# Kernel optimization log

Hardware: AMD Instinct MI355X
Metric: run time of the kernel (lower is better)

## Reference

```python
import jax, jax.numpy as jnp
import numpy as np
import math

D = 128      # out_dim (= d)
H = 4        # n_heads
DK = D // H  # d_k = 32
M = 5        # fixed num types in forward
NN = 15      # fixed N in forward
SQRT_DK = math.sqrt(DK)


def setup_inputs() -> dict:
    key = jax.random.key(0)
    ks = jax.random.split(key, 18)
    b, n = 1024, 64
    inp = {
        "node_inp": jax.random.normal(ks[0], (D, b, n), jnp.float32),
        "WW": jax.random.normal(ks[1], (b, M, n, NN), jnp.float32) * 0.1,
        "mask_matrix": jax.random.uniform(ks[2], (M * NN, n), jnp.float32),
        "R": jax.random.normal(ks[3], (b, H, n, n), jnp.float32),
        "attn_mask": jax.random.uniform(ks[4], (1, 1, n, 4 * n), jnp.float32),
        # learned parameters (xavier-ish scale)
        "WK": jax.random.normal(ks[5], (M, D, D), jnp.float32) * 0.05,
        "bK": jax.random.normal(ks[6], (M, D, 1), jnp.float32) * 0.05,
        "WQ": jax.random.normal(ks[7], (M, D, D), jnp.float32) * 0.05,
        "bQ": jax.random.normal(ks[8], (M, D, 1), jnp.float32) * 0.05,
        "WM": jax.random.normal(ks[9], (M, D, D), jnp.float32) * 0.05,
        "bM": jax.random.normal(ks[10], (M, D, 1), jnp.float32) * 0.05,
        "WB": jax.random.normal(ks[11], (M, D, D), jnp.float32) * 0.05,
        "bB": jax.random.normal(ks[12], (M, D, 1), jnp.float32) * 0.05,
        "Wmsgup": jax.random.normal(ks[13], (DK, DK), jnp.float32) * 0.1,
        "Wmsgdown": jax.random.normal(ks[14], (DK, DK), jnp.float32) * 0.1,
        "Wmsgleft": jax.random.normal(ks[15], (DK, DK), jnp.float32) * 0.1,
        "Wmsgright": jax.random.normal(ks[16], (DK, DK), jnp.float32) * 0.1,
    }
    return inp


def reference(node_inp, WW, mask_matrix, R, attn_mask,
              WK, bK, WQ, bQ, WM, bM, WB, bB,
              Wmsgup, Wmsgdown, Wmsgleft, Wmsgright):
    d, b, n = node_inp.shape
    # project node features through per-type mixing: (b, m, d, N)
    node_inp_m = jnp.einsum('dbn,bmnN->bmdN', node_inp, WW)

    def proj_perm(W, bias):
        # per-type linear then permute(0,2,1,3) before flatten (as K/Q do)
        x = jnp.einsum('mde,bmeN->bmdN', W, node_inp_m) + bias[None]  # (b,m,d,N)
        x = x.transpose(0, 2, 1, 3).reshape(b, d, M * NN)
        return x @ mask_matrix  # (b, d, n)

    K = proj_perm(WK, bK).reshape(b, H, DK, n)
    Q = proj_perm(WQ, bQ).reshape(b, H, DK, n)

    # message: NOTE original reshapes (b*m,d,N) -> (b,d,m*N) WITHOUT the permute; replicate faithfully
    msg = jnp.einsum('mde,bmeN->bmdN', WM, node_inp_m) + bM[None]  # (b,m,d,N)
    message = msg.reshape(b, d, M * NN) @ mask_matrix               # (b, d, n)

    A = jnp.einsum('bhki,bhkj->bhij', Q, K) / SQRT_DK               # (b,h,n,n)
    aw = jax.nn.softmax(R + A, axis=3)
    aw = jnp.where(jnp.isnan(aw), jnp.zeros_like(aw), aw)
    aw = jnp.tile(aw, (1, 1, 1, 4)) * attn_mask                     # (b,h,n,4n)

    res_msg = message.reshape(b, H, DK, n)
    Wmsg = jnp.concatenate([Wmsgup, Wmsgdown, Wmsgleft, Wmsgright], axis=1)  # (dk, 4dk)
    res = jnp.einsum('kq,bhkn->bhqn', Wmsg, res_msg)                # (b,h,4dk,n)
    res = res.reshape(b, H, DK, 4 * n)                               # faithful reshape

    B = jnp.einsum('bhnm,bhkm->bhkn', aw, res).reshape(b, d, n)
    B = jax.nn.gelu(B, approximate=False)

    Bm = jnp.einsum('bdn,bmnN->bmdN', B, WW)
    Bm = jnp.einsum('mde,bmeN->bmdN', WB, Bm) + bB[None]
    Bm = Bm.transpose(0, 2, 1, 3).reshape(b, d, M * NN) @ mask_matrix  # (b,d,n)
    out = Bm.transpose(1, 0, 2) + node_inp                             # (d,b,n)
    return (out, aw[0, 0])
```

## Files before the change

### kernel.cpp

```cpp
#include <hip/hip_runtime.h>
#include <math.h>

#define Dd 128
#define Hh 4
#define DKk 32
#define Mm 5
#define NNn 15
#define Bb 1024
#define Nn 64
#define MN 75
#define BN 65536
#define RSQRT_DK 0.17677669529663687f

typedef __attribute__((ext_vector_type(8))) short bf16x8;
typedef __attribute__((ext_vector_type(4))) float f32x4;

__device__ __forceinline__ ushort f2bf(float x) {
    unsigned u = __float_as_uint(x);
    u = (u + 0x7fffu + ((u >> 16) & 1u)) >> 16;
    return (ushort)u;
}
__device__ __forceinline__ float bf2f(ushort h) {
    return __uint_as_float(((unsigned)h) << 16);
}
__device__ __forceinline__ void split2(float x, ushort& hi, ushort& lo) {
    hi = f2bf(x);
    lo = f2bf(x - bf2f(hi));
}
__device__ __forceinline__ f32x4 MFMA(bf16x8 a, bf16x8 b, f32x4 c) {
    return __builtin_amdgcn_mfma_f32_16x16x32_bf16(a, b, c, 0, 0, 0);
}

__global__ void k0_prep(const float* __restrict__ maskm,
                        const float* __restrict__ WK, const float* __restrict__ bK,
                        const float* __restrict__ WQ, const float* __restrict__ bQ,
                        const float* __restrict__ WM, const float* __restrict__ bM,
                        const float* __restrict__ WB, const float* __restrict__ bB,
                        const float* __restrict__ Wu, const float* __restrict__ Wd,
                        const float* __restrict__ Wl, const float* __restrict__ Wr,
                        ushort* __restrict__ WKhi, ushort* __restrict__ WKlo,
                        ushort* __restrict__ WQhi, ushort* __restrict__ WQlo,
                        ushort* __restrict__ WMhi, ushort* __restrict__ WBhi,
                        ushort* __restrict__ maskhi, ushort* __restrict__ masklo,
                        ushort* __restrict__ maskThi, ushort* __restrict__ maskTlo,
                        float* __restrict__ btKT, float* __restrict__ btQT,
                        float* __restrict__ btMT, float* __restrict__ btB,
                        ushort* __restrict__ WcatT)
{
    int tid = blockIdx.x * blockDim.x + threadIdx.x;
    int nthr = gridDim.x * blockDim.x;
    const int NW = Mm * Dd * Dd;
    for (int i = tid; i < NW; i += nthr) {
        split2(WK[i], WKhi[i], WKlo[i]);
        split2(WQ[i], WQhi[i], WQlo[i]);
        WMhi[i] = f2bf(WM[i]);
        WBhi[i] = f2bf(WB[i]);
    }
    for (int i = tid; i < 96 * 64; i += nthr) {
        float v = (i < MN * 64) ? maskm[i] : 0.f;
        split2(v, maskhi[i], masklo[i]);
    }
    for (int i = tid; i < 64 * 96; i += nthr) {
        int col = i / 96, j = i - col * 96;
        float v = (j < MN) ? maskm[j * 64 + col] : 0.f;
        split2(v, maskThi[i], maskTlo[i]);
    }
    for (int i = tid; i < 4096; i += nthr) {
        int q = i >> 5, kk = i & 31;
        const float* Wsel = (q < 32) ? Wu : (q < 64) ? Wd : (q < 96) ? Wl : Wr;
        WcatT[i] = f2bf(Wsel[kk * 32 + (q & 31)]);
    }
    for (int i = tid; i < 8192; i += nthr) {
        int d = i >> 6, col = i & 63;
        float aKv = 0.f, aQv = 0.f, aBv = 0.f;
        for (int m = 0; m < Mm; ++m) {
            float mrs = 0.f;
            for (int N = 0; N < NNn; ++N) mrs += maskm[(m * 15 + N) * 64 + col];
            aKv += bK[m * 128 + d] * mrs;
            aQv += bQ[m * 128 + d] * mrs;
            aBv += bB[m * 128 + d] * mrs;
        }
        btKT[col * 128 + d] = aKv;
        btQT[col * 128 + d] = aQv;
        btB[i] = aBv;
        float aMv = 0.f;
        for (int j = 0; j < MN; ++j) {
            int f = d * 75 + j;
            int m = f / 1920;
            int dloc = (f / 15) & 127;
            aMv += bM[m * 128 + dloc] * maskm[j * 64 + col];
        }
        btMT[col * 128 + d] = aMv;
    }
}

__global__ __launch_bounds__(512, 4) void k1_proj(
    const float* __restrict__ node, const float* __restrict__ WW,
    const ushort* __restrict__ WKhi, const ushort* __restrict__ WKlo,
    const ushort* __restrict__ WQhi, const ushort* __restrict__ WQlo,
    const ushort* __restrict__ WMhi,
    const ushort* __restrict__ maskThi, const ushort* __restrict__ maskTlo,
    const float* __restrict__ btKT, const float* __restrict__ btQT,
    const float* __restrict__ btMT,
    ushort* __restrict__ Khi, ushort* __restrict__ Klo,
    ushort* __restrict__ Qhi, ushort* __restrict__ Qlo,
    ushort* __restrict__ msgTg)
{
    const int b = blockIdx.x;
    const int tid = threadIdx.x;
    const int lane = tid & 63, w = tid >> 6;
    const int l15 = lane & 15, lq = lane >> 4;

    __shared__ ushort nimTh[80 * 136];
    __shared__ ushort nimTl[80 * 136];
    __shared__ ushort planes[4 * 32 * 104];

    ushort* Ykh = planes;
    ushort* Ykl = planes + 32 * 104;
    ushort* Yqh = planes + 2 * 32 * 104;
    ushort* Yql = planes + 3 * 32 * 104;

    for (int t = tid; t < 5 * 136; t += 512) {
        int mm = t / 136, e = t - mm * 136;
        nimTh[(mm * 16 + 15) * 136 + e] = 0;
        nimTl[(mm * 16 + 15) * 136 + e] = 0;
    }
    for (int t = tid; t < 128 * 29; t += 512) {
        int r = t / 29, cc = 75 + (t - r * 29);
        planes[r * 104 + cc] = 0;
    }

    const f32x4 zz = {0.f, 0.f, 0.f, 0.f};

    {
        bf16x8 ah[2], al[2];
        #pragma unroll
        for (int ks = 0; ks < 2; ++ks) {
            const float* np = node + (size_t)(w * 16 + l15) * BN + b * 64 + ks * 32 + lq * 8;
            float tmp[8];
            *(float4*)tmp       = *(const float4*)np;
            *(float4*)(tmp + 4) = *(const float4*)(np + 4);
            #pragma unroll
            for (int j = 0; j < 8; ++j) {
                ushort h_, l_; split2(tmp[j], h_, l_);
                ah[ks][j] = (short)h_; al[ks][j] = (short)l_;
            }
        }
        for (int m = 0; m < Mm; ++m) {
            const float* wp = WW + ((size_t)b * Mm + m) * 960 + (l15 < 15 ? l15 : 0);
            f32x4 chh = zz, chl = zz, clh = zz;
            #pragma unroll
            for (int ks = 0; ks < 2; ++ks) {
                bf16x8 bh, bl;
                #pragma unroll
                for (int t = 0; t < 8; ++t) {
                    int n = ks * 32 + lq * 8 + t;
                    float v = (l15 < 15) ? wp[n * 15] : 0.f;
                    ushort h_, l_; split2(v, h_, l_);
                    bh[t] = (short)h_; bl[t] = (short)l_;
                }
                chh = MFMA(ah[ks], bh, chh);
                chl = MFMA(ah[ks], bl, chl);
                clh = MFMA(al[ks], bh, clh);
            }
            f32x4 c = chh + chl + clh;
            if (l15 < 15) {
                #pragma unroll
                for (int t = 0; t < 4; ++t) {
                    int e = w * 16 + lq * 4 + t;
                    split2(c[t], nimTh[(m * 16 + l15) * 136 + e],
                                 nimTl[(m * 16 + l15) * 136 + e]);
                }
            }
        }
    }
    __syncthreads();

    for (int qd = 0; qd < 4; ++qd) {
        for (int u = w; u < 10; u += 8) {
            int m = u >> 1, rt = u & 1;
            int d0 = qd * 32 + rt * 16 + l15;
            f32x4 khh = zz, khl = zz, klh = zz;
            f32x4 qhh = zz, qhl = zz, qlh = zz;
            #pragma unroll
            for (int ks = 0; ks < 4; ++ks) {
                int k0 = ks * 32 + lq * 8;
                size_t wo = (size_t)m * 16384 + (size_t)d0 * 128 + k0;
                bf16x8 akh = *(const bf16x8*)(WKhi + wo);
                bf16x8 akl = *(const bf16x8*)(WKlo + wo);
                bf16x8 aqh = *(const bf16x8*)(WQhi + wo);
                bf16x8 aql = *(const bf16x8*)(WQlo + wo);
                bf16x8 bh = *(const bf16x8*)(&nimTh[(m * 16 + l15) * 136 + k0]);
                bf16x8 bl = *(const bf16x8*)(&nimTl[(m * 16 + l15) * 136 + k0]);
                khh = MFMA(akh, bh, khh); khl = MFMA(akh, bl, khl); klh = MFMA(akl, bh, klh);
                qhh = MFMA(aqh, bh, qhh); qhl = MFMA(aqh, bl, qhl); qlh = MFMA(aql, bh, qlh);
            }
            f32x4 cK = khh + khl + klh;
            f32x4 cQ = qhh + qhl + qlh;
            if (l15 < 15) {
                int j = m * 15 + l15;
                #pragma unroll
                for (int t = 0; t < 4; ++t) {
                    int r = rt * 16 + lq * 4 + t;
                    split2(cK[t], Ykh[r * 104 + j], Ykl[r * 104 + j]);
                    split2(cQ[t], Yqh[r * 104 + j], Yql[r * 104 + j]);
                }
            }
        }
        __syncthreads();
        {
            int nr = w & 3, dc = w >> 2;
            f32x4 khh = zz, khl = zz, klh = zz;
            f32x4 qhh = zz, qhl = zz, qlh = zz;
            #pragma unroll
            for (int ks = 0; ks < 3; ++ks) {
                int k0 = ks * 32 + lq * 8;
                bf16x8 mh = *(const bf16x8*)(maskThi + (nr * 16 + l15) * 96 + k0);
                bf16x8 ml = *(const bf16x8*)(maskTlo + (nr * 16 + l15) * 96 + k0);
                bf16x8 ykh = *(const bf16x8*)(&Ykh[(dc * 16 + l15) * 104 + k0]);
                bf16x8 ykl = *(const bf16x8*)(&Ykl[(dc * 16 + l15) * 104 + k0]);
                bf16x8 yqh = *(const bf16x8*)(&Yqh[(dc * 16 + l15) * 104 + k0]);
                bf16x8 yql = *(const bf16x8*)(&Yql[(dc * 16 + l15) * 104 + k0]);
                khh = MFMA(mh, ykh, khh); khl = MFMA(ml, ykh, khl); klh = MFMA(mh, ykl, klh);
                qhh = MFMA(mh, yqh, qhh); qhl = MFMA(ml, yqh, qhl); qlh = MFMA(mh, yql, qlh);
            }
            f32x4 cK = khh + khl + klh;
            f32x4 cQ = qhh + qhl + qlh;
            #pragma unroll
            for (int t = 0; t < 4; ++t) {
                int n = nr * 16 + lq * 4 + t;
                int dloc = dc * 16 + l15;
                int d = qd * 32 + dloc;
                size_t oi = (((size_t)(b * 4 + qd)) * 64 + n) * 32 + dloc;
                ushort hh_, ll_;
                split2(cK[t] + btKT[n * 128 + d], hh_, ll_);
                Khi[oi] = hh_; Klo[oi] = ll_;
                split2(cQ[t] + btQT[n * 128 + d], hh_, ll_);
                Qhi[oi] = hh_; Qlo[oi] = ll_;
            }
        }
        __syncthreads();
    }

    {
        int rt = w;
        for (int m = 0; m < Mm; ++m) {
            f32x4 c0 = zz, c1 = zz;
            #pragma unroll
            for (int ks = 0; ks < 4; ++ks) {
                int k0 = ks * 32 + lq * 8;
                bf16x8 a  = *(const bf16x8*)(WMhi + (size_t)m * 16384 + (size_t)(rt * 16 + l15) * 128 + k0);
                bf16x8 bh = *(const bf16x8*)(&nimTh[(m * 16 + l15) * 136 + k0]);
                if (ks < 2) c0 = MFMA(a, bh, c0); else c1 = MFMA(a, bh, c1);
            }
            f32x4 c = c0 + c1;
            if (l15 < 15) {
                #pragma unroll
                for (int t = 0; t < 4; ++t) {
                    int dflat = rt * 16 + lq * 4 + t;
                    int g = m * 1920 + dflat * 15 + l15;
                    planes[(g / 75) * 104 + (g % 75)] = f2bf(c[t]);
                }
            }
        }
    }
    __syncthreads();
    #pragma unroll
    for (int s = 0; s < 4; ++s) {
        int u = w * 4 + s;
        int nr = u & 3, ddc = u >> 2;
        f32x4 cs0 = zz, cs1 = zz, cs2 = zz;
        {
            bf16x8 a0 = *(const bf16x8*)(maskThi + (nr * 16 + l15) * 96 + lq * 8);
            bf16x8 b0 = *(const bf16x8*)(&planes[(ddc * 16 + l15) * 104 + lq * 8]);
            cs0 = MFMA(a0, b0, cs0);
            bf16x8 a1 = *(const bf16x8*)(maskThi + (nr * 16 + l15) * 96 + 32 + lq * 8);
            bf16x8 b1 = *(const bf16x8*)(&planes[(ddc * 16 + l15) * 104 + 32 + lq * 8]);
            cs1 = MFMA(a1, b1, cs1);
            bf16x8 a2 = *(const bf16x8*)(maskThi + (nr * 16 + l15) * 96 + 64 + lq * 8);
            bf16x8 b2 = *(const bf16x8*)(&planes[(ddc * 16 + l15) * 104 + 64 + lq * 8]);
            cs2 = MFMA(a2, b2, cs2);
        }
        f32x4 c = cs0 + cs1 + cs2;
        #pragma unroll
        for (int t = 0; t < 4; ++t) {
            int n = nr * 16 + lq * 4 + t;
            int dd = ddc * 16 + l15;
            int h = dd >> 5, dk = dd & 31;
            msgTg[(((size_t)(b * 4 + h)) * 64 + n) * 32 + dk] = f2bf(c[t] + btMT[n * 128 + dd]);
        }
    }
}

__global__ __launch_bounds__(512, 4) void k2_attn(
    const ushort* __restrict__ Khi, const ushort* __restrict__ Klo,
    const ushort* Qhi, const ushort* __restrict__ Qlo,
    const ushort* __restrict__ msgTg,
    const float* __restrict__ R, const float* __restrict__ am,
    const ushort* __restrict__ WcatT, float* __restrict__ aw00,
    ushort* Bout)
{
    const int b = blockIdx.x >> 2, h = blockIdx.x & 3;
    const int tid = threadIdx.x;
    const int lane = tid & 63, w = tid >> 6;
    const int l15 = lane & 15, lq = lane >> 4;

    __shared__ float  ST[64 * 65];
    __shared__ ushort resS[128 * 72];
    __shared__ ushort awq[64 * 72];

    const f32x4 zz = {0.f, 0.f, 0.f, 0.f};
    const size_t base2 = (size_t)(b * 4 + h) * 2048;
    const float* Rb = R + (size_t)(b * 4 + h) * 4096;

    {
        int ti = w >> 1;
        bf16x8 ah = *(const bf16x8*)(Qhi + base2 + (size_t)(ti * 16 + l15) * 32 + lq * 8);
        bf16x8 al = *(const bf16x8*)(Qlo + base2 + (size_t)(ti * 16 + l15) * 32 + lq * 8);
        #pragma unroll
        for (int s = 0; s < 2; ++s) {
            int tj = (w & 1) * 2 + s;
            bf16x8 bh = *(const bf16x8*)(Khi + base2 + (size_t)(tj * 16 + l15) * 32 + lq * 8);
            bf16x8 bl = *(const bf16x8*)(Klo + base2 + (size_t)(tj * 16 + l15) * 32 + lq * 8);
            f32x4 chh = zz, chl = zz, clh = zz;
            chh = MFMA(ah, bh, chh); chl = MFMA(ah, bl, chl); clh = MFMA(al, bh, clh);
            f32x4 c = chh + chl + clh;
            #pragma unroll
            for (int r = 0; r < 4; ++r) {
                int i = ti * 16 + lq * 4 + r, j = tj * 16 + l15;
                ST[j * 65 + i] = Rb[i * 64 + j] + c[r] * RSQRT_DK;
            }
        }
    }
    {
        bf16x8 a = *(const bf16x8*)(WcatT + (w * 16 + l15) * 32 + lq * 8);
        #pragma unroll
        for (int nt = 0; nt < 4; ++nt) {
            bf16x8 bfr = *(const bf16x8*)(msgTg + base2 + (size_t)(nt * 16 + l15) * 32 + lq * 8);
            f32x4 c = MFMA(a, bfr, zz);
            #pragma unroll
            for (int r = 0; r < 4; ++r)
                resS[(w * 16 + lq * 4 + r) * 72 + nt * 16 + l15] = f2bf(c[r]);
        }
    }
    __syncthreads();

    {
        int row = tid >> 3, part = tid & 7;
        float v[8]; float mx = -INFINITY;
        #pragma unroll
        for (int jj = 0; jj < 8; ++jj) { v[jj] = ST[(part * 8 + jj) * 65 + row]; mx = fmaxf(mx, v[jj]); }
        mx = fmaxf(mx, __shfl_xor(mx, 1));
        mx = fmaxf(mx, __shfl_xor(mx, 2));
        mx = fmaxf(mx, __shfl_xor(mx, 4));
        float s = 0.f;
        #pragma unroll
        for (int jj = 0; jj < 8; ++jj) { v[jj] = expf(v[jj] - mx); s += v[jj]; }
        s += __shfl_xor(s, 1); s += __shfl_xor(s, 2); s += __shfl_xor(s, 4);
        float inv = 1.f / s;
        #pragma unroll
        for (int jj = 0; jj < 8; ++jj) {
            float p = v[jj] * inv;
            ST[(part * 8 + jj) * 65 + row] = isnan(p) ? 0.f : p;
        }
    }
    __syncthreads();

    const int kt = w >> 2, it = w & 3;
    f32x4 accB0 = zz, accB1 = zz;
    for (int q = 0; q < 4; ++q) {
        for (int e = tid; e < 4096; e += 512) {
            int i = e >> 6, j0 = e & 63;
            float p = ST[j0 * 65 + i] * am[i * 256 + q * 64 + j0];
            awq[i * 72 + j0] = f2bf(p);
            if (blockIdx.x == 0) aw00[i * 256 + q * 64 + j0] = p;
        }
        __syncthreads();
        int row = 4 * (kt * 16 + l15) + q;
        bf16x8 a0 = *(const bf16x8*)(&resS[row * 72 + lq * 8]);
        bf16x8 b0 = *(const bf16x8*)(&awq[(it * 16 + l15) * 72 + lq * 8]);
        accB0 = MFMA(a0, b0, accB0);
        bf16x8 a1 = *(const bf16x8*)(&resS[row * 72 + 32 + lq * 8]);
        bf16x8 b1 = *(const bf16x8*)(&awq[(it * 16 + l15) * 72 + 32 + lq * 8]);
        accB1 = MFMA(a1, b1, accB1);
        __syncthreads();
    }
    f32x4 accB = accB0 + accB1;

    #pragma unroll
    for (int r = 0; r < 4; ++r) {
        int k = kt * 16 + lq * 4 + r, i = it * 16 + l15;
        float x = accB[r];
        float g = 0.5f * x * (1.f + erff(x * 0.70710678118654752f));
        Bout[base2 + k * 64 + i] = f2bf(g);
    }
}

__global__ __launch_bounds__(512, 4) void k3_out(
    const ushort* Bbuf, const float* __restrict__ WW,
    const ushort* __restrict__ WBhi, const ushort* __restrict__ maskhi,
    const float* __restrict__ btB, const float* __restrict__ node,
    float* __restrict__ outp)
{
    const int b = blockIdx.x, tid = threadIdx.x;
    const int lane = tid & 63, w = tid >> 6, l15 = lane & 15, lq = lane >> 4;
    __shared__ ushort sB[128 * 72];
    __shared__ ushort wwh[64 * 17];
    __shared__ ushort t1[128 * 17];
    __shared__ ushort nm[32 * 66];

    for (int i = tid; i < 8192; i += 512) {
        int d = i >> 6, n = i & 63;
        sB[d * 72 + n] = Bbuf[(size_t)b * 8192 + i];
    }
    const f32x4 zz = {0.f, 0.f, 0.f, 0.f};
    f32x4 acc[4];
    for (int c = 0; c < 4; ++c) acc[c] = zz;
    __syncthreads();

    for (int m = 0; m < Mm; ++m) {
        for (int i = tid; i < 64 * 17; i += 512) {
            int n = i / 17, N = i - n * 17;
            wwh[i] = (N < 15) ? f2bf(WW[(((size_t)b * Mm + m) * 64 + n) * 15 + N]) : (ushort)0;
        }
        __syncthreads();
        {
            f32x4 c0 = zz, c1 = zz;
            #pragma unroll
            for (int ks = 0; ks < 2; ++ks) {
                int k0 = ks * 32 + (lq << 3);
                bf16x8 a = *(const bf16x8*)(&sB[(w * 16 + l15) * 72 + k0]);
                bf16x8 bh;
                #pragma unroll
                for (int t = 0; t < 8; ++t) bh[t] = (short)wwh[(k0 + t) * 17 + l15];
                if (ks == 0) c0 = MFMA(a, bh, c0); else c1 = MFMA(a, bh, c1);
            }
            f32x4 c = c0 + c1;
            #pragma unroll
            for (int t = 0; t < 4; ++t)
                t1[(w * 16 + lq * 4 + t) * 17 + l15] = f2bf(c[t]);
        }
        __syncthreads();

        bf16x8 mfh;
        {
            int ct = w & 3;
            int k0 = lq << 3;
            #pragma unroll
            for (int t = 0; t < 8; ++t) {
                int kk = k0 + t;
                int row = (kk < 15) ? (m * 15 + kk) : 95;
                mfh[t] = (short)maskhi[row * 64 + ct * 16 + l15];
            }
        }
        for (int eb = 0; eb < 4; ++eb) {
            {
                int rtl = w >> 2, ct = w & 3;
                int e = eb * 32 + rtl * 16 + l15;
                int k0 = lq << 3;
                bf16x8 a;
                #pragma unroll
                for (int t = 0; t < 8; ++t) {
                    int kk = k0 + t;
                    int cc = (kk < 15) ? kk : 15;
                    a[t] = (short)t1[e * 17 + cc];
                }
                f32x4 c = zz;
                c = MFMA(a, mfh, c);
                #pragma unroll
                for (int t = 0; t < 4; ++t)
                    nm[(rtl * 16 + lq * 4 + t) * 66 + ct * 16 + l15] = f2bf(c[t]);
            }
            __syncthreads();
            {
                size_t aoff = (size_t)(w * 16 + l15) * 128 + eb * 32 + (lq << 3);
                bf16x8 a = *(const bf16x8*)(WBhi + m * 16384 + aoff);
                int k0 = lq << 3;
                #pragma unroll
                for (int ct = 0; ct < 4; ++ct) {
                    bf16x8 bh;
                    #pragma unroll
                    for (int t = 0; t < 8; ++t) bh[t] = (short)nm[(k0 + t) * 66 + ct * 16 + l15];
                    acc[ct] = MFMA(a, bh, acc[ct]);
                }
            }
            __syncthreads();
        }
    }
    #pragma unroll
    for (int ct = 0; ct < 4; ++ct) {
        #pragma unroll
        for (int t = 0; t < 4; ++t) {
            int d = w * 16 + lq * 4 + t;
            int col = ct * 16 + l15;
            size_t gi = (size_t)d * BN + b * 64 + col;
            outp[gi] = acc[ct][t] + btB[d * 64 + col] + node[gi];
        }
    }
}

extern "C" void kernel_launch(void* const* d_in, const int* in_sizes, int n_in,
                              void* d_out, int out_size, void* d_ws, size_t ws_size,
                              hipStream_t stream) {
    const float* node  = (const float*)d_in[0];
    const float* WW    = (const float*)d_in[1];
    const float* maskm = (const float*)d_in[2];
    const float* R     = (const float*)d_in[3];
    const float* am    = (const float*)d_in[4];
    const float* WK = (const float*)d_in[5];  const float* bK = (const float*)d_in[6];
    const float* WQ = (const float*)d_in[7];  const float* bQ = (const float*)d_in[8];
    const float* WM = (const float*)d_in[9];  const float* bM = (const float*)d_in[10];
    const float* WB = (const float*)d_in[11]; const float* bB = (const float*)d_in[12];
    const float* Wu = (const float*)d_in[13]; const float* Wd = (const float*)d_in[14];
    const float* Wl = (const float*)d_in[15]; const float* Wr = (const float*)d_in[16];

    float* out  = (float*)d_out;
    float* aw00 = out + (size_t)Dd * BN;

    ushort* Khi = (ushort*)d_out;
    ushort* Klo = Khi + 8388608;

    char* W = (char*)d_ws;
    ushort* Qhi   = (ushort*)W;
    ushort* Qlo   = Qhi + 8388608;
    ushort* msgTg = Qlo + 8388608;
    ushort* WKhi  = msgTg + 8388608;
    ushort* WKlo  = WKhi + 81920;
    ushort* WQhi  = WKlo + 81920;
    ushort* WQlo  = WQhi + 81920;
    ushort* WMhi  = WQlo + 81920;
    ushort* WBhi  = WMhi + 81920;
    ushort* maskhi  = WBhi + 81920;
    ushort* masklo  = maskhi + 6144;
    ushort* maskThi = masklo + 6144;
    ushort* maskTlo = maskThi + 6144;
    ushort* WcatT   = maskTlo + 6144;
    float*  btKT = (float*)(WcatT + 4096);
    float*  btQT = btKT + 8192;
    float*  btMT = btQT + 8192;
    float*  btB  = btMT + 8192;

    k0_prep<<<512, 256, 0, stream>>>(maskm, WK, bK, WQ, bQ, WM, bM, WB, bB,
                                     Wu, Wd, Wl, Wr,
                                     WKhi, WKlo, WQhi, WQlo, WMhi, WBhi,
                                     maskhi, masklo, maskThi, maskTlo,
                                     btKT, btQT, btMT, btB, WcatT);
    k1_proj<<<Bb, 512, 0, stream>>>(node, WW, WKhi, WKlo, WQhi, WQlo, WMhi,
                                    maskThi, maskTlo, btKT, btQT, btMT,
                                    Khi, Klo, Qhi, Qlo, msgTg);
    k2_attn<<<Bb * Hh, 512, 0, stream>>>(Khi, Klo, Qhi, Qlo, msgTg, R, am,
                                         WcatT, aw00, Qhi );
    k3_out<<<Bb, 512, 0, stream>>>(Qhi , WW, WBhi, maskhi, btB, node, out);
}
```

Before: 279.7 us.

## Shrink k1 LDS footprint via swizzle, serialized K/Q passes, and buffer reuse

Reduces k1_proj shared memory by replacing padded node tiles with XOR-swizzled 128-wide rows, computing K and Q in two separate passes so only one pair of Y planes is needed, and reusing the low-half node buffer for the message plane. The launch bound is raised from 4 to 6 blocks per CU to exploit the lower LDS and register pressure. The cost is doubled passes with extra barriers and re-reading nimT tiles for Q, plus possible register spills under the tighter bound.

```diff
diff --git a/kernel.cpp b/kernel.cpp
--- a/kernel.cpp
+++ b/kernel.cpp
@@ -30,6 +30,8 @@
 __device__ __forceinline__ f32x4 MFMA(bf16x8 a, bf16x8 b, f32x4 c) {
     return __builtin_amdgcn_mfma_f32_16x16x32_bf16(a, b, c, 0, 0, 0);
 }
+
+#define NSWZ(r, c) ((r) * 128 + ((c) ^ (((r) & 7) << 3)))
 
 __global__ void k0_prep(const float* __restrict__ maskm,
                         const float* __restrict__ WK, const float* __restrict__ bK,
@@ -94,7 +96,7 @@
     }
 }
 
-__global__ __launch_bounds__(512, 4) void k1_proj(
+__global__ __launch_bounds__(512, 6) void k1_proj(
     const float* __restrict__ node, const float* __restrict__ WW,
     const ushort* __restrict__ WKhi, const ushort* __restrict__ WKlo,
     const ushort* __restrict__ WQhi, const ushort* __restrict__ WQlo,
@@ -111,26 +113,24 @@
     const int lane = tid & 63, w = tid >> 6;
     const int l15 = lane & 15, lq = lane >> 4;
 
-    __shared__ ushort nimTh[80 * 136];
-    __shared__ ushort nimTl[80 * 136];
-    __shared__ ushort planes[4 * 32 * 104];
-
-    ushort* Ykh = planes;
-    ushort* Ykl = planes + 32 * 104;
-    ushort* Yqh = planes + 2 * 32 * 104;
-    ushort* Yql = planes + 3 * 32 * 104;
-
-    for (int t = tid; t < 5 * 136; t += 512) {
-        int mm = t / 136, e = t - mm * 136;
-        nimTh[(mm * 16 + 15) * 136 + e] = 0;
-        nimTl[(mm * 16 + 15) * 136 + e] = 0;
-    }
-    for (int t = tid; t < 128 * 29; t += 512) {
+    __shared__ ushort nimTh[80 * 128];
+    __shared__ ushort nimTl[80 * 128];
+    __shared__ ushort Yh[32 * 104];
+    __shared__ ushort Yl[32 * 104];
+    ushort* xM = nimTl;
+
+    const f32x4 zz = {0.f, 0.f, 0.f, 0.f};
+
+    for (int t = tid; t < 5 * 128; t += 512) {
+        int mm = t >> 7, e = t & 127;
+        nimTh[(mm * 16 + 15) * 128 + e] = 0;
+        nimTl[(mm * 16 + 15) * 128 + e] = 0;
+    }
+    for (int t = tid; t < 32 * 29; t += 512) {
         int r = t / 29, cc = 75 + (t - r * 29);
-        planes[r * 104 + cc] = 0;
-    }
-
-    const f32x4 zz = {0.f, 0.f, 0.f, 0.f};
+        Yh[r * 104 + cc] = 0;
+        Yl[r * 104 + cc] = 0;
+    }
 
     {
         bf16x8 ah[2], al[2];
@@ -165,83 +165,83 @@
             }
             f32x4 c = chh + chl + clh;
             if (l15 < 15) {
+                int row = m * 16 + l15;
                 #pragma unroll
                 for (int t = 0; t < 4; ++t) {
                     int e = w * 16 + lq * 4 + t;
-                    split2(c[t], nimTh[(m * 16 + l15) * 136 + e],
-                                 nimTl[(m * 16 + l15) * 136 + e]);
+                    split2(c[t], nimTh[NSWZ(row, e)], nimTl[NSWZ(row, e)]);
                 }
             }
         }
     }
     __syncthreads();
 
-    for (int qd = 0; qd < 4; ++qd) {
-        for (int u = w; u < 10; u += 8) {
-            int m = u >> 1, rt = u & 1;
-            int d0 = qd * 32 + rt * 16 + l15;
-            f32x4 khh = zz, khl = zz, klh = zz;
-            f32x4 qhh = zz, qhl = zz, qlh = zz;
-            #pragma unroll
-            for (int ks = 0; ks < 4; ++ks) {
-                int k0 = ks * 32 + lq * 8;
-                size_t wo = (size_t)m * 16384 + (size_t)d0 * 128 + k0;
-                bf16x8 akh = *(const bf16x8*)(WKhi + wo);
-                bf16x8 akl = *(const bf16x8*)(WKlo + wo);
-                bf16x8 aqh = *(const bf16x8*)(WQhi + wo);
-                bf16x8 aql = *(const bf16x8*)(WQlo + wo);
-                bf16x8 bh = *(const bf16x8*)(&nimTh[(m * 16 + l15) * 136 + k0]);
-                bf16x8 bl = *(const bf16x8*)(&nimTl[(m * 16 + l15) * 136 + k0]);
-                khh = MFMA(akh, bh, khh); khl = MFMA(akh, bl, khl); klh = MFMA(akl, bh, klh);
-                qhh = MFMA(aqh, bh, qhh); qhl = MFMA(aqh, bl, qhl); qlh = MFMA(aql, bh, qlh);
-            }
-            f32x4 cK = khh + khl + klh;
-            f32x4 cQ = qhh + qhl + qlh;
-            if (l15 < 15) {
-                int j = m * 15 + l15;
+    for (int P = 0; P < 2; ++P) {
+        const ushort* Whi = P ? WQhi : WKhi;
+        const ushort* Wlo = P ? WQlo : WKlo;
+        const float*  btP = P ? btQT : btKT;
+        ushort* Phi = P ? Qhi : Khi;
+        ushort* Plo = P ? Qlo : Klo;
+
+        for (int qd = 0; qd < 4; ++qd) {
+            for (int u = w; u < 10; u += 8) {
+                int m = u >> 1, rt = u & 1;
+                int d0 = qd * 32 + rt * 16 + l15;
+                f32x4 phh = zz, phl = zz, plh = zz;
+                #pragma unroll
+                for (int ks = 0; ks < 4; ++ks) {
+                    int k0 = ks * 32 + lq * 8;
+                    size_t wo = (size_t)m * 16384 + (size_t)d0 * 128 + k0;
+                    bf16x8 awh = *(const bf16x8*)(Whi + wo);
+                    bf16x8 awl = *(const bf16x8*)(Wlo + wo);
+                    int nrow = m * 16 + l15;
+                    bf16x8 bh = *(const bf16x8*)(&nimTh[NSWZ(nrow, k0)]);
+                    bf16x8 bl = *(const bf16x8*)(&nimTl[NSWZ(nrow, k0)]);
+                    phh = MFMA(awh, bh, phh); phl = MFMA(awh, bl, phl); plh = MFMA(awl, bh, plh);
+                }
+                f32x4 c = phh + phl + plh;
+                if (l15 < 15) {
+                    int j = m * 15 + l15;
+                    #pragma unroll
+                    for (int t = 0; t < 4; ++t) {
+                        int r = rt * 16 + lq * 4 + t;
+                        split2(c[t], Yh[r * 104 + j], Yl[r * 104 + j]);
+                    }
+                }
+            }
+            __syncthreads();
+            {
+                int nr = w & 3, dc = w >> 2;
+                f32x4 phh = zz, phl = zz, plh = zz;
+                #pragma unroll
+                for (int ks = 0; ks < 3; ++ks) {
+                    int k0 = ks * 32 + lq * 8;
+                    bf16x8 mh = *(const bf16x8*)(maskThi + (nr * 16 + l15) * 96 + k0);
+                    bf16x8 ml = *(const bf16x8*)(maskTlo + (nr * 16 + l15) * 96 + k0);
+                    bf16x8 yh = *(const bf16x8*)(&Yh[(dc * 16 + l15) * 104 + k0]);
+                    bf16x8 yl = *(const bf16x8*)(&Yl[(dc * 16 + l15) * 104 + k0]);
+                    phh = MFMA(mh, yh, phh); phl = MFMA(ml, yh, phl); plh = MFMA(mh, yl, plh);
+                }
+                f32x4 c = phh + phl + plh;
                 #pragma unroll
                 for (int t = 0; t < 4; ++t) {
-                    int r = rt * 16 + lq * 4 + t;
-                    split2(cK[t], Ykh[r * 104 + j], Ykl[r * 104 + j]);
-                    split2(cQ[t], Yqh[r * 104 + j], Yql[r * 104 + j]);
-                }
-            }
-        }
-        __syncthreads();
-        {
-            int nr = w & 3, dc = w >> 2;
-            f32x4 khh = zz, khl = zz, klh = zz;
-            f32x4 qhh = zz, qhl = zz, qlh = zz;
-            #pragma unroll
-            for (int ks = 0; ks < 3; ++ks) {
-                int k0 = ks * 32 + lq * 8;
-                bf16x8 mh = *(const bf16x8*)(maskThi + (nr * 16 + l15) * 96 + k0);
-                bf16x8 ml = *(const bf16x8*)(maskTlo + (nr * 16 + l15) * 96 + k0);
-                bf16x8 ykh = *(const bf16x8*)(&Ykh[(dc * 16 + l15) * 104 + k0]);
-                bf16x8 ykl = *(const bf16x8*)(&Ykl[(dc * 16 + l15) * 104 + k0]);
-                bf16x8 yqh = *(const bf16x8*)(&Yqh[(dc * 16 + l15) * 104 + k0]);
-                bf16x8 yql = *(const bf16x8*)(&Yql[(dc * 16 + l15) * 104 + k0]);
-                khh = MFMA(mh, ykh, khh); khl = MFMA(ml, ykh, khl); klh = MFMA(mh, ykl, klh);
-                qhh = MFMA(mh, yqh, qhh); qhl = MFMA(ml, yqh, qhl); qlh = MFMA(mh, yql, qlh);
-            }
-            f32x4 cK = khh + khl + klh;
-            f32x4 cQ = qhh + qhl + qlh;
-            #pragma unroll
-            for (int t = 0; t < 4; ++t) {
-                int n = nr * 16 + lq * 4 + t;
-                int dloc = dc * 16 + l15;
-                int d = qd * 32 + dloc;
-                size_t oi = (((size_t)(b * 4 + qd)) * 64 + n) * 32 + dloc;
-                ushort hh_, ll_;
-                split2(cK[t] + btKT[n * 128 + d], hh_, ll_);
-                Khi[oi] = hh_; Klo[oi] = ll_;
-                split2(cQ[t] + btQT[n * 128 + d], hh_, ll_);
-                Qhi[oi] = hh_; Qlo[oi] = ll_;
-            }
-        }
-        __syncthreads();
-    }
-
+                    int n = nr * 16 + lq * 4 + t;
+                    int dloc = dc * 16 + l15;
+                    int d = qd * 32 + dloc;
+                    size_t oi = (((size_t)(b * 4 + qd)) * 64 + n) * 32 + dloc;
+                    ushort hh_, ll_;
+                    split2(c[t] + btP[n * 128 + d], hh_, ll_);
+                    Phi[oi] = hh_; Plo[oi] = ll_;
+                }
+            }
+            __syncthreads();
+        }
+    }
+
+    for (int t = tid; t < 128 * 5; t += 512) {
+        int r = t / 5, cc = 75 + (t - r * 5);
+        xM[r * 80 + cc] = 0;
+    }
     {
         int rt = w;
         for (int m = 0; m < Mm; ++m) {
@@ -250,7 +250,8 @@
             for (int ks = 0; ks < 4; ++ks) {
                 int k0 = ks * 32 + lq * 8;
                 bf16x8 a  = *(const bf16x8*)(WMhi + (size_t)m * 16384 + (size_t)(rt * 16 + l15) * 128 + k0);
-                bf16x8 bh = *(const bf16x8*)(&nimTh[(m * 16 + l15) * 136 + k0]);
+                int nrow = m * 16 + l15;
+                bf16x8 bh = *(const bf16x8*)(&nimTh[NSWZ(nrow, k0)]);
                 if (ks < 2) c0 = MFMA(a, bh, c0); else c1 = MFMA(a, bh, c1);
             }
             f32x4 c = c0 + c1;
@@ -259,7 +260,7 @@
                 for (int t = 0; t < 4; ++t) {
                     int dflat = rt * 16 + lq * 4 + t;
                     int g = m * 1920 + dflat * 15 + l15;
-                    planes[(g / 75) * 104 + (g % 75)] = f2bf(c[t]);
+                    xM[(g / 75) * 80 + (g % 75)] = f2bf(c[t]);
                 }
             }
         }
@@ -272,13 +273,13 @@
         f32x4 cs0 = zz, cs1 = zz, cs2 = zz;
         {
             bf16x8 a0 = *(const bf16x8*)(maskThi + (nr * 16 + l15) * 96 + lq * 8);
-            bf16x8 b0 = *(const bf16x8*)(&planes[(ddc * 16 + l15) * 104 + lq * 8]);
+            bf16x8 b0 = *(const bf16x8*)(&xM[(ddc * 16 + l15) * 80 + lq * 8]);
             cs0 = MFMA(a0, b0, cs0);
             bf16x8 a1 = *(const bf16x8*)(maskThi + (nr * 16 + l15) * 96 + 32 + lq * 8);
-            bf16x8 b1 = *(const bf16x8*)(&planes[(ddc * 16 + l15) * 104 + 32 + lq * 8]);
+            bf16x8 b1 = *(const bf16x8*)(&xM[(ddc * 16 + l15) * 80 + 32 + lq * 8]);
             cs1 = MFMA(a1, b1, cs1);
             bf16x8 a2 = *(const bf16x8*)(maskThi + (nr * 16 + l15) * 96 + 64 + lq * 8);
-            bf16x8 b2 = *(const bf16x8*)(&planes[(ddc * 16 + l15) * 104 + 64 + lq * 8]);
+            bf16x8 b2 = *(const bf16x8*)(&xM[(ddc * 16 + l15) * 80 + 64 + lq * 8]);
             cs2 = MFMA(a2, b2, cs2);
         }
         f32x4 c = cs0 + cs1 + cs2;
```

New measurement: 319.2 us. 14.1% more time.

## Split projection kernel into nim, K/Q, and message kernels via global staging

Applied to the files above, without the earlier changes.

The monolithic per-batch projection kernel is split into three kernels. The first computes the WW-mixed node features and stores their hi/lo bf16 parts to a new global workspace. The second computes K/Q with one block per (batch, quarter), giving four times more blocks and smaller LDS use. The third computes the message projection. This is meant to raise occupancy and parallelism and shrink per-block LDS, at the cost of a large global round trip for the intermediate features (about 40 MB) and two extra launches.

```diff
diff --git a/kernel.cpp b/kernel.cpp
--- a/kernel.cpp
+++ b/kernel.cpp
@@ -94,49 +94,28 @@
     }
 }
 
-__global__ __launch_bounds__(512, 4) void k1_proj(
+__global__ __launch_bounds__(256, 6) void k1a_nim(
     const float* __restrict__ node, const float* __restrict__ WW,
-    const ushort* __restrict__ WKhi, const ushort* __restrict__ WKlo,
-    const ushort* __restrict__ WQhi, const ushort* __restrict__ WQlo,
-    const ushort* __restrict__ WMhi,
-    const ushort* __restrict__ maskThi, const ushort* __restrict__ maskTlo,
-    const float* __restrict__ btKT, const float* __restrict__ btQT,
-    const float* __restrict__ btMT,
-    ushort* __restrict__ Khi, ushort* __restrict__ Klo,
-    ushort* __restrict__ Qhi, ushort* __restrict__ Qlo,
-    ushort* __restrict__ msgTg)
+    ushort* __restrict__ nimHg, ushort* __restrict__ nimLg)
 {
     const int b = blockIdx.x;
     const int tid = threadIdx.x;
     const int lane = tid & 63, w = tid >> 6;
     const int l15 = lane & 15, lq = lane >> 4;
-
-    __shared__ ushort nimTh[80 * 136];
-    __shared__ ushort nimTl[80 * 136];
-    __shared__ ushort planes[4 * 32 * 104];
-
-    ushort* Ykh = planes;
-    ushort* Ykl = planes + 32 * 104;
-    ushort* Yqh = planes + 2 * 32 * 104;
-    ushort* Yql = planes + 3 * 32 * 104;
-
-    for (int t = tid; t < 5 * 136; t += 512) {
-        int mm = t / 136, e = t - mm * 136;
-        nimTh[(mm * 16 + 15) * 136 + e] = 0;
-        nimTl[(mm * 16 + 15) * 136 + e] = 0;
-    }
-    for (int t = tid; t < 128 * 29; t += 512) {
-        int r = t / 29, cc = 75 + (t - r * 29);
-        planes[r * 104 + cc] = 0;
-    }
-
     const f32x4 zz = {0.f, 0.f, 0.f, 0.f};
 
-    {
+    for (int t = tid; t < 5 * 128; t += 256) {
+        int mm = t >> 7, e = t & 127;
+        nimHg[(size_t)b * 10240 + (mm * 16 + 15) * 128 + e] = 0;
+        nimLg[(size_t)b * 10240 + (mm * 16 + 15) * 128 + e] = 0;
+    }
+
+    for (int s = 0; s < 2; ++s) {
+        int eb = w * 2 + s;
         bf16x8 ah[2], al[2];
         #pragma unroll
         for (int ks = 0; ks < 2; ++ks) {
-            const float* np = node + (size_t)(w * 16 + l15) * BN + b * 64 + ks * 32 + lq * 8;
+            const float* np = node + (size_t)(eb * 16 + l15) * BN + b * 64 + ks * 32 + lq * 8;
             float tmp[8];
             *(float4*)tmp       = *(const float4*)np;
             *(float4*)(tmp + 4) = *(const float4*)(np + 4);
@@ -165,92 +144,143 @@
             }
             f32x4 c = chh + chl + clh;
             if (l15 < 15) {
-                #pragma unroll
-                for (int t = 0; t < 4; ++t) {
-                    int e = w * 16 + lq * 4 + t;
-                    split2(c[t], nimTh[(m * 16 + l15) * 136 + e],
-                                 nimTl[(m * 16 + l15) * 136 + e]);
-                }
+                int row = m * 16 + l15;
+                ushort h0, h1, h2, h3, l0, l1, l2, l3;
+                split2(c[0], h0, l0); split2(c[1], h1, l1);
+                split2(c[2], h2, l2); split2(c[3], h3, l3);
+                size_t base = (size_t)b * 10240 + row * 128 + eb * 16 + lq * 4;
+                *(unsigned*)(nimHg + base)     = (unsigned)h0 | ((unsigned)h1 << 16);
+                *(unsigned*)(nimHg + base + 2) = (unsigned)h2 | ((unsigned)h3 << 16);
+                *(unsigned*)(nimLg + base)     = (unsigned)l0 | ((unsigned)l1 << 16);
+                *(unsigned*)(nimLg + base + 2) = (unsigned)l2 | ((unsigned)l3 << 16);
+            }
+        }
+    }
+}
+
+__global__ __launch_bounds__(256, 6) void k1b_kq(
+    const ushort* __restrict__ nimHg, const ushort* __restrict__ nimLg,
+    const ushort* __restrict__ WKhi, const ushort* __restrict__ WKlo,
+    const ushort* __restrict__ WQhi, const ushort* __restrict__ WQlo,
+    const ushort* __restrict__ maskThi, const ushort* __restrict__ maskTlo,
+    const float* __restrict__ btKT, const float* __restrict__ btQT,
+    ushort* __restrict__ Khi, ushort* __restrict__ Klo,
+    ushort* __restrict__ Qhi, ushort* __restrict__ Qlo)
+{
+    const int b = blockIdx.x >> 2, qd = blockIdx.x & 3;
+    const int tid = threadIdx.x;
+    const int lane = tid & 63, w = tid >> 6;
+    const int l15 = lane & 15, lq = lane >> 4;
+
+    __shared__ ushort Ykh[32 * 104], Ykl[32 * 104];
+    __shared__ ushort Yqh[32 * 104], Yql[32 * 104];
+
+    const f32x4 zz = {0.f, 0.f, 0.f, 0.f};
+    const size_t nbase = (size_t)b * 10240;
+
+    for (int t = tid; t < 32 * 29; t += 256) {
+        int r = t / 29, cc = 75 + (t - r * 29);
+        Ykh[r * 104 + cc] = 0; Ykl[r * 104 + cc] = 0;
+        Yqh[r * 104 + cc] = 0; Yql[r * 104 + cc] = 0;
+    }
+
+    for (int u = w; u < 10; u += 4) {
+        int m = u >> 1, rt = u & 1;
+        int d0 = qd * 32 + rt * 16 + l15;
+        f32x4 khh = zz, khl = zz, klh = zz;
+        f32x4 qhh = zz, qhl = zz, qlh = zz;
+        #pragma unroll
+        for (int ks = 0; ks < 4; ++ks) {
+            int k0 = ks * 32 + lq * 8;
+            size_t wo = (size_t)m * 16384 + (size_t)d0 * 128 + k0;
+            bf16x8 akh = *(const bf16x8*)(WKhi + wo);
+            bf16x8 akl = *(const bf16x8*)(WKlo + wo);
+            bf16x8 aqh = *(const bf16x8*)(WQhi + wo);
+            bf16x8 aql = *(const bf16x8*)(WQlo + wo);
+            bf16x8 bh = *(const bf16x8*)(nimHg + nbase + (m * 16 + l15) * 128 + k0);
+            bf16x8 bl = *(const bf16x8*)(nimLg + nbase + (m * 16 + l15) * 128 + k0);
+            khh = MFMA(akh, bh, khh); khl = MFMA(akh, bl, khl); klh = MFMA(akl, bh, klh);
+            qhh = MFMA(aqh, bh, qhh); qhl = MFMA(aqh, bl, qhl); qlh = MFMA(aql, bh, qlh);
+        }
+        f32x4 cK = khh + khl + klh;
+        f32x4 cQ = qhh + qhl + qlh;
+        if (l15 < 15) {
+            int j = m * 15 + l15;
+            #pragma unroll
+            for (int t = 0; t < 4; ++t) {
+                int r = rt * 16 + lq * 4 + t;
+                split2(cK[t], Ykh[r * 104 + j], Ykl[r * 104 + j]);
+                split2(cQ[t], Yqh[r * 104 + j], Yql[r * 104 + j]);
             }
         }
     }
     __syncthreads();
 
-    for (int qd = 0; qd < 4; ++qd) {
-        for (int u = w; u < 10; u += 8) {
-            int m = u >> 1, rt = u & 1;
-            int d0 = qd * 32 + rt * 16 + l15;
-            f32x4 khh = zz, khl = zz, klh = zz;
-            f32x4 qhh = zz, qhl = zz, qlh = zz;
-            #pragma unroll
-            for (int ks = 0; ks < 4; ++ks) {
-                int k0 = ks * 32 + lq * 8;
-                size_t wo = (size_t)m * 16384 + (size_t)d0 * 128 + k0;
-                bf16x8 akh = *(const bf16x8*)(WKhi + wo);
-                bf16x8 akl = *(const bf16x8*)(WKlo + wo);
-                bf16x8 aqh = *(const bf16x8*)(WQhi + wo);
-                bf16x8 aql = *(const bf16x8*)(WQlo + wo);
-                bf16x8 bh = *(const bf16x8*)(&nimTh[(m * 16 + l15) * 136 + k0]);
-                bf16x8 bl = *(const bf16x8*)(&nimTl[(m * 16 + l15) * 136 + k0]);
-                khh = MFMA(akh, bh, khh); khl = MFMA(akh, bl, khl); klh = MFMA(akl, bh, klh);
-                qhh = MFMA(aqh, bh, qhh); qhl = MFMA(aqh, bl, qhl); qlh = MFMA(aql, bh, qlh);
-            }
-            f32x4 cK = khh + khl + klh;
-            f32x4 cQ = qhh + qhl + qlh;
-            if (l15 < 15) {
-                int j = m * 15 + l15;
-                #pragma unroll
-                for (int t = 0; t < 4; ++t) {
-                    int r = rt * 16 + lq * 4 + t;
-                    split2(cK[t], Ykh[r * 104 + j], Ykl[r * 104 + j]);
-                    split2(cQ[t], Yqh[r * 104 + j], Yql[r * 104 + j]);
-                }
-            }
-        }
-        __syncthreads();
-        {
-            int nr = w & 3, dc = w >> 2;
-            f32x4 khh = zz, khl = zz, klh = zz;
-            f32x4 qhh = zz, qhl = zz, qlh = zz;
-            #pragma unroll
-            for (int ks = 0; ks < 3; ++ks) {
-                int k0 = ks * 32 + lq * 8;
-                bf16x8 mh = *(const bf16x8*)(maskThi + (nr * 16 + l15) * 96 + k0);
-                bf16x8 ml = *(const bf16x8*)(maskTlo + (nr * 16 + l15) * 96 + k0);
-                bf16x8 ykh = *(const bf16x8*)(&Ykh[(dc * 16 + l15) * 104 + k0]);
-                bf16x8 ykl = *(const bf16x8*)(&Ykl[(dc * 16 + l15) * 104 + k0]);
-                bf16x8 yqh = *(const bf16x8*)(&Yqh[(dc * 16 + l15) * 104 + k0]);
-                bf16x8 yql = *(const bf16x8*)(&Yql[(dc * 16 + l15) * 104 + k0]);
-                khh = MFMA(mh, ykh, khh); khl = MFMA(ml, ykh, khl); klh = MFMA(mh, ykl, klh);
-                qhh = MFMA(mh, yqh, qhh); qhl = MFMA(ml, yqh, qhl); qlh = MFMA(mh, yql, qlh);
-            }
-            f32x4 cK = khh + khl + klh;
-            f32x4 cQ = qhh + qhl + qlh;
-            #pragma unroll
-            for (int t = 0; t < 4; ++t) {
-                int n = nr * 16 + lq * 4 + t;
-                int dloc = dc * 16 + l15;
-                int d = qd * 32 + dloc;
-                size_t oi = (((size_t)(b * 4 + qd)) * 64 + n) * 32 + dloc;
-                ushort hh_, ll_;
-                split2(cK[t] + btKT[n * 128 + d], hh_, ll_);
-                Khi[oi] = hh_; Klo[oi] = ll_;
-                split2(cQ[t] + btQT[n * 128 + d], hh_, ll_);
-                Qhi[oi] = hh_; Qlo[oi] = ll_;
-            }
-        }
-        __syncthreads();
-    }
-
-    {
-        int rt = w;
+    #pragma unroll
+    for (int s = 0; s < 2; ++s) {
+        int u = w * 2 + s;
+        int nr = u & 3, dc = u >> 2;
+        f32x4 khh = zz, khl = zz, klh = zz;
+        f32x4 qhh = zz, qhl = zz, qlh = zz;
+        #pragma unroll
+        for (int ks = 0; ks < 3; ++ks) {
+            int k0 = ks * 32 + lq * 8;
+            bf16x8 mh = *(const bf16x8*)(maskThi + (nr * 16 + l15) * 96 + k0);
+            bf16x8 ml = *(const bf16x8*)(maskTlo + (nr * 16 + l15) * 96 + k0);
+            bf16x8 ykh = *(const bf16x8*)(&Ykh[(dc * 16 + l15) * 104 + k0]);
+            bf16x8 ykl = *(const bf16x8*)(&Ykl[(dc * 16 + l15) * 104 + k0]);
+            bf16x8 yqh = *(const bf16x8*)(&Yqh[(dc * 16 + l15) * 104 + k0]);
+            bf16x8 yql = *(const bf16x8*)(&Yql[(dc * 16 + l15) * 104 + k0]);
+            khh = MFMA(mh, ykh, khh); khl = MFMA(ml, ykh, khl); klh = MFMA(mh, ykl, klh);
+            qhh = MFMA(mh, yqh, qhh); qhl = MFMA(ml, yqh, qhl); qlh = MFMA(mh, yql, qlh);
+        }
+        f32x4 cK = khh + khl + klh;
+        f32x4 cQ = qhh + qhl + qlh;
+        #pragma unroll
+        for (int t = 0; t < 4; ++t) {
+            int n = nr * 16 + lq * 4 + t;
+            int dloc = dc * 16 + l15;
+            int d = qd * 32 + dloc;
+            size_t oi = (((size_t)(b * 4 + qd)) * 64 + n) * 32 + dloc;
+            ushort hh_, ll_;
+            split2(cK[t] + btKT[n * 128 + d], hh_, ll_);
+            Khi[oi] = hh_; Klo[oi] = ll_;
+            split2(cQ[t] + btQT[n * 128 + d], hh_, ll_);
+            Qhi[oi] = hh_; Qlo[oi] = ll_;
+        }
+    }
+}
+
+__global__ __launch_bounds__(256, 6) void k1c_msg(
+    const ushort* __restrict__ nimHg,
+    const ushort* __restrict__ WMhi, const ushort* __restrict__ maskThi,
+    const float* __restrict__ btMT, ushort* __restrict__ msgTg)
+{
+    const int b = blockIdx.x;
+    const int tid = threadIdx.x;
+    const int lane = tid & 63, w = tid >> 6;
+    const int l15 = lane & 15, lq = lane >> 4;
+
+    __shared__ __align__(16) ushort xM[128 * 80 + 16];
+
+    const f32x4 zz = {0.f, 0.f, 0.f, 0.f};
+    const size_t nbase = (size_t)b * 10240;
+
+    for (int t = tid; t < 128 * 5; t += 256) {
+        int r = t / 5, cc = 75 + (t - r * 5);
+        xM[r * 80 + cc] = 0;
+    }
+    if (tid < 16) xM[10240 + tid] = 0;
+
+    for (int s = 0; s < 2; ++s) {
+        int rt = w * 2 + s;
         for (int m = 0; m < Mm; ++m) {
             f32x4 c0 = zz, c1 = zz;
             #pragma unroll
             for (int ks = 0; ks < 4; ++ks) {
                 int k0 = ks * 32 + lq * 8;
                 bf16x8 a  = *(const bf16x8*)(WMhi + (size_t)m * 16384 + (size_t)(rt * 16 + l15) * 128 + k0);
-                bf16x8 bh = *(const bf16x8*)(&nimTh[(m * 16 + l15) * 136 + k0]);
+                bf16x8 bh = *(const bf16x8*)(nimHg + nbase + (m * 16 + l15) * 128 + k0);
                 if (ks < 2) c0 = MFMA(a, bh, c0); else c1 = MFMA(a, bh, c1);
             }
             f32x4 c = c0 + c1;
@@ -259,26 +289,27 @@
                 for (int t = 0; t < 4; ++t) {
                     int dflat = rt * 16 + lq * 4 + t;
                     int g = m * 1920 + dflat * 15 + l15;
-                    planes[(g / 75) * 104 + (g % 75)] = f2bf(c[t]);
+                    xM[(g / 75) * 80 + (g % 75)] = f2bf(c[t]);
                 }
             }
         }
     }
     __syncthreads();
+
     #pragma unroll
-    for (int s = 0; s < 4; ++s) {
-        int u = w * 4 + s;
+    for (int s2 = 0; s2 < 8; ++s2) {
+        int u = w * 8 + s2;
         int nr = u & 3, ddc = u >> 2;
         f32x4 cs0 = zz, cs1 = zz, cs2 = zz;
         {
             bf16x8 a0 = *(const bf16x8*)(maskThi + (nr * 16 + l15) * 96 + lq * 8);
-            bf16x8 b0 = *(const bf16x8*)(&planes[(ddc * 16 + l15) * 104 + lq * 8]);
+            bf16x8 b0 = *(const bf16x8*)(&xM[(ddc * 16 + l15) * 80 + lq * 8]);
             cs0 = MFMA(a0, b0, cs0);
             bf16x8 a1 = *(const bf16x8*)(maskThi + (nr * 16 + l15) * 96 + 32 + lq * 8);
-            bf16x8 b1 = *(const bf16x8*)(&planes[(ddc * 16 + l15) * 104 + 32 + lq * 8]);
+            bf16x8 b1 = *(const bf16x8*)(&xM[(ddc * 16 + l15) * 80 + 32 + lq * 8]);
             cs1 = MFMA(a1, b1, cs1);
             bf16x8 a2 = *(const bf16x8*)(maskThi + (nr * 16 + l15) * 96 + 64 + lq * 8);
-            bf16x8 b2 = *(const bf16x8*)(&planes[(ddc * 16 + l15) * 104 + 64 + lq * 8]);
+            bf16x8 b2 = *(const bf16x8*)(&xM[(ddc * 16 + l15) * 80 + 64 + lq * 8]);
             cs2 = MFMA(a2, b2, cs2);
         }
         f32x4 c = cs0 + cs1 + cs2;
@@ -524,7 +555,9 @@
     ushort* Qhi   = (ushort*)W;
     ushort* Qlo   = Qhi + 8388608;
     ushort* msgTg = Qlo + 8388608;
-    ushort* WKhi  = msgTg + 8388608;
+    ushort* nimHg = msgTg + 8388608;
+    ushort* nimLg = nimHg + 10485760;
+    ushort* WKhi  = nimLg + 10485760;
     ushort* WKlo  = WKhi + 81920;
     ushort* WQhi  = WKlo + 81920;
     ushort* WQlo  = WQhi + 81920;
@@ -545,9 +578,11 @@
                                      WKhi, WKlo, WQhi, WQlo, WMhi, WBhi,
                                      maskhi, masklo, maskThi, maskTlo,
                                      btKT, btQT, btMT, btB, WcatT);
-    k1_proj<<<Bb, 512, 0, stream>>>(node, WW, WKhi, WKlo, WQhi, WQlo, WMhi,
-                                    maskThi, maskTlo, btKT, btQT, btMT,
-                                    Khi, Klo, Qhi, Qlo, msgTg);
+    k1a_nim<<<Bb, 256, 0, stream>>>(node, WW, nimHg, nimLg);
+    k1b_kq<<<Bb * 4, 256, 0, stream>>>(nimHg, nimLg, WKhi, WKlo, WQhi, WQlo,
+                                       maskThi, maskTlo, btKT, btQT,
+                                       Khi, Klo, Qhi, Qlo);
+    k1c_msg<<<Bb, 256, 0, stream>>>(nimHg, WMhi, maskThi, btMT, msgTg);
     k2_attn<<<Bb * Hh, 512, 0, stream>>>(Khi, Klo, Qhi, Qlo, msgTg, R, am,
                                          WcatT, aw00, Qhi );
     k3_out<<<Bb, 512, 0, stream>>>(Qhi , WW, WBhi, maskhi, btB, node, out);
```

Measured after the change: 367.0 us. 31.2% more time.
